# Optimization experiments

Hardware: AMD Instinct MI355X
Metric: run time of the kernel (lower is better)

## Reference

```python
import jax, jax.numpy as jnp
import numpy as np

BETA = 1.0
DEPTH = 10
LEVELS = DEPTH - 1          # decision levels along any root->leaf path
NUM_LEAVES = 2 ** LEVELS    # 512
NUM_INTERNAL = NUM_LEAVES - 1  # 511, heap-ordered: root=0, children 2i+1/2i+2


def _tree_paths():
    """For each leaf, the heap indices of its ancestors and the branch taken (0=left,1=right)."""
    anc = np.zeros((NUM_LEAVES, LEVELS), dtype=np.int32)
    bits = np.zeros((NUM_LEAVES, LEVELS), dtype=np.int32)
    for j in range(NUM_LEAVES):
        node = 0
        for t in range(LEVELS):
            bit = (j >> (LEVELS - 1 - t)) & 1
            anc[j, t] = node
            bits[j, t] = bit
            node = 2 * node + 1 + bit
    return jnp.asarray(anc), jnp.asarray(bits)

_ANC, _BITS = _tree_paths()


def setup_inputs() -> dict:
    key = jax.random.key(0)
    k1, k2, k3, k4 = jax.random.split(key, 4)
    B, F, K = 8192, 4096, 1000
    return {
        "xs": jax.random.normal(k1, (B, F), dtype=jnp.float32),
        "W": jax.random.normal(k2, (NUM_INTERNAL, F), dtype=jnp.float32) * (1.0 / np.sqrt(F)),
        "b": jax.random.normal(k3, (NUM_INTERNAL,), dtype=jnp.float32) * 0.01,
        "leaf_params": jax.random.normal(k4, (NUM_LEAVES, K), dtype=jnp.float32),
    }


def reference(xs, W, b, leaf_params):
    # All node projections as one GEMM: [B, NUM_INTERNAL]
    ps = jax.nn.sigmoid(BETA * (xs @ W.T + b))
    # Gather per-leaf ancestor probs: [B, NUM_LEAVES, LEVELS]
    g = ps[:, _ANC]
    edge = jnp.where(_BITS[None] == 1, g, 1.0 - g)
    leaf_prob = jnp.prod(edge, axis=-1)          # [B, NUM_LEAVES]
    dists = jax.nn.softmax(leaf_params, axis=-1)  # [NUM_LEAVES, K]
    return leaf_prob @ dists                      # [B, K]
```

## Files before the change

kernel.cpp:

```cpp
#include <hip/hip_runtime.h>


typedef __bf16 bf16x8 __attribute__((ext_vector_type(8)));
typedef float f32x4 __attribute__((ext_vector_type(4)));
typedef _Float16 f16x8 __attribute__((ext_vector_type(8)));

#define B_DIM 8192
#define F_DIM 4096
#define NI 511
#define NL 512
#define K_DIM 1000
#define KPAD 1024
#define SPLIT 3

#define W_BLKS  1024
#define SM_BLKS 512

__device__ inline unsigned short f2bf(float f) {
    unsigned int u = __float_as_uint(f);
    return (unsigned short)((u + 0x7FFFu + ((u >> 16) & 1u)) >> 16);
}
__device__ inline unsigned int pk_bf16(float a, float b) {
    return (unsigned int)f2bf(a) | ((unsigned int)f2bf(b) << 16);
}
__device__ inline unsigned int pk2_hu(float a, float b) {
    unsigned int ua = __float_as_uint(a) + 0x8000u;
    unsigned int ub = __float_as_uint(b) + 0x8000u;
    return __builtin_amdgcn_perm(ub, ua, 0x07060302u);
}

typedef __attribute__((address_space(1))) const unsigned int guint;
typedef __attribute__((address_space(3))) unsigned int luint;
__device__ inline void gload16(const unsigned short* g, unsigned short* l) {
    __builtin_amdgcn_global_load_lds((guint*)g, (luint*)l, 16, 0, 0);
}

__device__ inline bf16x8 ldb(const unsigned short* Lbase, int r, int kb) {
    const int g = (kb >> 3) ^ (r & 7);
    return *(const bf16x8*)&Lbase[r * 64 + g * 8];
}

__device__ inline float waveMax(float v) {
#pragma unroll
    for (int off = 32; off; off >>= 1) v = fmaxf(v, __shfl_down(v, off, 64));
    return v;
}
__device__ inline float waveSum(float v) {
#pragma unroll
    for (int off = 32; off; off >>= 1) v += __shfl_down(v, off, 64);
    return v;
}

__global__ __launch_bounds__(256) void prep_kernel(
    const float* __restrict__ W, unsigned short* __restrict__ Wb,
    const float* __restrict__ lp, unsigned short* __restrict__ dT)
{
    __shared__ float sred[8];
    const int bid = blockIdx.x;
    const int tid = threadIdx.x;

    if (bid < W_BLKS) {
        const size_t i = ((size_t)bid * 256 + tid) * 8;
        const int row = (int)(i >> 12);
        uint4 h = {0u, 0u, 0u, 0u};
        if (row < NI) {
            const float4 a = *(const float4*)(W + i);
            const float4 b = *(const float4*)(W + i + 4);
            h.x = pk_bf16(a.x, a.y);
            h.y = pk_bf16(a.z, a.w);
            h.z = pk_bf16(b.x, b.y);
            h.w = pk_bf16(b.z, b.w);
        }
        *(uint4*)(Wb + i) = h;
        return;
    }
    const int k = bid - W_BLKS;
    const int lane = tid & 63;
    const int wave = tid >> 6;
    const float* rowp = lp + (size_t)k * K_DIM;

    float vals[4];
    float mx = -3.0e38f;
#pragma unroll
    for (int c = 0; c < 4; ++c) {
        const int n = tid + c * 256;
        vals[c] = (n < K_DIM) ? rowp[n] : -3.0e38f;
        mx = fmaxf(mx, vals[c]);
    }
    mx = waveMax(mx);
    if (lane == 0) sred[wave] = mx;
    __syncthreads();
    const float gmax = fmaxf(fmaxf(sred[0], sred[1]), fmaxf(sred[2], sred[3]));

    float sum = 0.f;
#pragma unroll
    for (int c = 0; c < 4; ++c) {
        const int n = tid + c * 256;
        const float e = (n < K_DIM) ? __expf(vals[c] - gmax) : 0.f;
        vals[c] = e;
        sum += e;
    }
    sum = waveSum(sum);
    if (lane == 0) sred[4 + wave] = sum;
    __syncthreads();
    const float inv = 1.0f / (sred[4] + sred[5] + sred[6] + sred[7]);
#pragma unroll
    for (int c = 0; c < 4; ++c) {
        const int n = tid + c * 256;
        if (n < K_DIM) dT[(size_t)n * NL + k] = f2bf(vals[c] * inv);
    }
}

__global__ __launch_bounds__(256) __attribute__((amdgpu_waves_per_eu(3, 3)))
void gemm1_kernel(
    const float* __restrict__ A, const unsigned short* __restrict__ Bb,
    _Float16* __restrict__ part)
{
    __shared__ __align__(16) unsigned short Al[128 * 64];
    __shared__ __align__(16) unsigned short Bl[2][128 * 64];

    const int id = blockIdx.x;
    const int xcd = id & 7;
    const int j = id >> 3;
    const int nt = j & 3;
    const int rem = j >> 2;
    const int mhi = rem / 3;
    const int z = rem - mhi * 3;
    const int m0 = (mhi * 8 + xcd) * 128;
    const int n0 = nt * 128;
    const int kbeg = z * 1408;
    const int NT = (z == 2) ? 20 : 22;

    const int tid = threadIdx.x;
    const int lane = tid & 63;
    const int wave = tid >> 6;
    const int wm = (wave >> 1) * 64;
    const int wn = (wave & 1) * 64;
    const int quad = lane >> 4;
    const int l16 = lane & 15;

    const int rowA = wave * 4 + (lane >> 4);
    const int q = lane & 15;
    const float* gA = A + (size_t)(m0 + rowA) * F_DIM + kbeg + q * 4;
    unsigned short* lw[8];
#pragma unroll
    for (int p = 0; p < 8; ++p) {
        const int r = rowA + p * 16;
        lw[p] = &Al[r * 64 + (((q >> 1) ^ (r & 7)) * 8) + (q & 1) * 4];
    }

    const int drb = lane >> 3;
    const int cb = ((lane & 7) ^ drb) * 8;
    const unsigned short* gB = Bb + (size_t)(n0 + wave * 8 + drb) * F_DIM + kbeg + cb;
    const int lBoff = wave * 8 * 64;

    const f32x4 zero = {0.f, 0.f, 0.f, 0.f};
    f32x4 acc[4][4];
#pragma unroll
    for (int i = 0; i < 4; ++i)
#pragma unroll
        for (int j2 = 0; j2 < 4; ++j2) acc[i][j2] = zero;

    f32x4 abf[8];
    uint2 abh[8];

#pragma unroll
    for (int p = 0; p < 4; ++p)
        gload16(gB + (size_t)p * 32 * F_DIM, &Bl[0][lBoff + p * 2048]);
    __builtin_amdgcn_sched_barrier(0);
#pragma unroll
    for (int p = 0; p < 8; ++p)
        abf[p] = *(const f32x4*)(gA + (size_t)p * 16 * F_DIM);
    __builtin_amdgcn_sched_barrier(0);
#pragma unroll
    for (int p = 0; p < 8; ++p) {
        abh[p].x = pk2_hu(abf[p].x, abf[p].y);
        abh[p].y = pk2_hu(abf[p].z, abf[p].w);
    }
#pragma unroll
    for (int p = 0; p < 8; ++p)
        abf[p] = *(const f32x4*)(gA + 64 + (size_t)p * 16 * F_DIM);
    __builtin_amdgcn_sched_barrier(0);

    for (int t = 0; t < NT; ++t) {
#pragma unroll
        for (int p = 0; p < 8; ++p)
            *(uint2*)lw[p] = abh[p];
        if (t < NT - 1) {
            asm volatile("s_waitcnt vmcnt(8) lgkmcnt(0)" ::: "memory");
        } else {
            asm volatile("s_waitcnt vmcnt(0) lgkmcnt(0)" ::: "memory");
        }
        __builtin_amdgcn_sched_barrier(0);
        __builtin_amdgcn_s_barrier();
        __builtin_amdgcn_sched_barrier(0);
        if (t + 1 < NT) {
#pragma unroll
            for (int p = 0; p < 4; ++p)
                gload16(gB + (size_t)(t + 1) * 64 + (size_t)p * 32 * F_DIM,
                        &Bl[(t + 1) & 1][lBoff + p * 2048]);
        }
        __builtin_amdgcn_sched_barrier(0);
        if (t + 1 < NT) {
#pragma unroll
            for (int p = 0; p < 8; ++p) {
                abh[p].x = pk2_hu(abf[p].x, abf[p].y);
                abh[p].y = pk2_hu(abf[p].z, abf[p].w);
            }
        }
        if (t + 2 < NT) {
#pragma unroll
            for (int p = 0; p < 8; ++p)
                abf[p] = *(const f32x4*)(gA + (size_t)(t + 2) * 64
                                         + (size_t)p * 16 * F_DIM);
        }
        __builtin_amdgcn_sched_barrier(0);
        const unsigned short* Bcur = &Bl[t & 1][0];
#pragma unroll
        for (int kk = 0; kk < 64; kk += 32) {
            const int kb = kk + quad * 8;
            bf16x8 av[4], bv[4];
#pragma unroll
            for (int i = 0; i < 4; ++i)
                av[i] = ldb(Al, wm + i * 16 + l16, kb);
#pragma unroll
            for (int j2 = 0; j2 < 4; ++j2)
                bv[j2] = ldb(Bcur, wn + j2 * 16 + l16, kb);
#pragma unroll
            for (int i = 0; i < 4; ++i)
#pragma unroll
                for (int j2 = 0; j2 < 4; ++j2)
                    acc[i][j2] = __builtin_amdgcn_mfma_f32_16x16x32_bf16(
                        av[i], bv[j2], acc[i][j2], 0, 0, 0);
        }
        __builtin_amdgcn_sched_barrier(0);
        __builtin_amdgcn_s_barrier();
        __builtin_amdgcn_sched_barrier(0);
    }

    _Float16* dst = part + (size_t)z * ((size_t)B_DIM * NL);
#pragma unroll
    for (int i = 0; i < 4; ++i) {
        const int mbase = m0 + wm + i * 16 + quad * 4;
#pragma unroll
        for (int j2 = 0; j2 < 4; ++j2) {
            const int n = n0 + wn + j2 * 16 + l16;
#pragma unroll
            for (int r = 0; r < 4; ++r)
                dst[(size_t)(mbase + r) * NL + n] = (_Float16)acc[i][j2][r];
        }
    }
}

__global__ __launch_bounds__(256) void reduce_tree_kernel(
    const _Float16* __restrict__ part, const float* __restrict__ bvec,
    unsigned short* __restrict__ leafbf)
{
    __shared__ float bsh[NL];
    __shared__ float prow[4][NL];

    const int tid = threadIdx.x;
    bsh[tid] = (tid < NI) ? bvec[tid] : 0.0f;
    const int t2 = tid + 256;
    bsh[t2] = (t2 < NI) ? bvec[t2] : 0.0f;

    const int wave = tid >> 6;
    const int lane = tid & 63;
    const int row = blockIdx.x * 4 + wave;
    const size_t base = (size_t)row * NL + lane * 8;

    float v[8] = {0.f, 0.f, 0.f, 0.f, 0.f, 0.f, 0.f, 0.f};
#pragma unroll
    for (int s = 0; s < SPLIT; ++s) {
        const f16x8 h = *(const f16x8*)(part + (size_t)s * ((size_t)B_DIM * NL) + base);
#pragma unroll
        for (int e = 0; e < 8; ++e) v[e] += (float)h[e];
    }
    __syncthreads();

#pragma unroll
    for (int i = 0; i < 8; ++i) {
        const float x = v[i] + bsh[lane * 8 + i];
        prow[wave][lane * 8 + i] = 1.0f / (1.0f + __expf(-x));
    }
    __syncthreads();

    const float* pr = prow[wave];
    float pre = 1.0f;
    int pnode = 0;
#pragma unroll
    for (int t = 5; t >= 0; --t) {
        const int bit = (lane >> t) & 1;
        const float p = pr[pnode];
        pre *= bit ? p : (1.0f - p);
        pnode = 2 * pnode + 1 + bit;
    }
    unsigned short outs[8];
#pragma unroll
    for (int jj = 0; jj < 8; ++jj) {
        float prob = pre;
        int node = pnode;
#pragma unroll
        for (int t = 2; t >= 0; --t) {
            const int bit = (jj >> t) & 1;
            const float p = pr[node];
            prob *= bit ? p : (1.0f - p);
            node = 2 * node + 1 + bit;
        }
        outs[jj] = f2bf(prob);
    }
    uint4 r;
    r.x = (unsigned int)outs[0] | ((unsigned int)outs[1] << 16);
    r.y = (unsigned int)outs[2] | ((unsigned int)outs[3] << 16);
    r.z = (unsigned int)outs[4] | ((unsigned int)outs[5] << 16);
    r.w = (unsigned int)outs[6] | ((unsigned int)outs[7] << 16);
    *(uint4*)(leafbf + (size_t)row * NL + lane * 8) = r;
}

__global__ __launch_bounds__(256, 2) void gemm2_kernel(
    const unsigned short* __restrict__ A, const unsigned short* __restrict__ Bm,
    float* __restrict__ out)
{
    __shared__ __align__(16) unsigned short Al[2][128 * 64];
    __shared__ __align__(16) unsigned short Bl[2][128 * 64];

    const int id = blockIdx.x;
    const int xcd = id & 7;
    const int j = id >> 3;
    const int nt = j & 7;
    const int mhi = j >> 3;
    const int m0 = (mhi * 8 + xcd) * 128;
    const int n0 = nt * 128;

    const int tid = threadIdx.x;
    const int lane = tid & 63;
    const int wave = tid >> 6;
    const int wm = (wave >> 1) * 64;
    const int wn = (wave & 1) * 64;
    const int quad = lane >> 4;
    const int l16 = lane & 15;

    const int drb = lane >> 3;
    const int cb = ((lane & 7) ^ drb) * 8;
    const unsigned short* gA = A + (size_t)(m0 + wave * 8 + drb) * NL + cb;
    const unsigned short* gB = Bm + (size_t)(n0 + wave * 8 + drb) * NL + cb;
    const int loff = wave * 8 * 64;

    const f32x4 zero = {0.f, 0.f, 0.f, 0.f};
    f32x4 acc[4][4];
#pragma unroll
    for (int i = 0; i < 4; ++i)
#pragma unroll
        for (int j2 = 0; j2 < 4; ++j2) acc[i][j2] = zero;

#pragma unroll
    for (int p = 0; p < 4; ++p) {
        gload16(gA + (size_t)p * 32 * NL, &Al[0][loff + p * 2048]);
        gload16(gB + (size_t)p * 32 * NL, &Bl[0][loff + p * 2048]);
    }
    __builtin_amdgcn_sched_barrier(0);

#pragma unroll
    for (int t = 0; t < 8; ++t) {
        if (t + 1 < 8) {
#pragma unroll
            for (int p = 0; p < 4; ++p) {
                gload16(gA + (size_t)(t + 1) * 64 + (size_t)p * 32 * NL,
                        &Al[(t + 1) & 1][loff + p * 2048]);
                gload16(gB + (size_t)(t + 1) * 64 + (size_t)p * 32 * NL,
                        &Bl[(t + 1) & 1][loff + p * 2048]);
            }
            __builtin_amdgcn_sched_barrier(0);
            asm volatile("s_waitcnt vmcnt(8)" ::: "memory");
        } else {
            __builtin_amdgcn_sched_barrier(0);
            asm volatile("s_waitcnt vmcnt(0)" ::: "memory");
        }
        __builtin_amdgcn_sched_barrier(0);
        __builtin_amdgcn_s_barrier();
        __builtin_amdgcn_sched_barrier(0);
#pragma unroll
        for (int kk = 0; kk < 64; kk += 32) {
            const int kb = kk + quad * 8;
            bf16x8 av[4], bv[4];
#pragma unroll
            for (int i = 0; i < 4; ++i)
                av[i] = ldb(&Al[t & 1][0], wm + i * 16 + l16, kb);
#pragma unroll
            for (int j2 = 0; j2 < 4; ++j2)
                bv[j2] = ldb(&Bl[t & 1][0], wn + j2 * 16 + l16, kb);
#pragma unroll
            for (int i = 0; i < 4; ++i)
#pragma unroll
                for (int j2 = 0; j2 < 4; ++j2)
                    acc[i][j2] = __builtin_amdgcn_mfma_f32_16x16x32_bf16(av[i], bv[j2], acc[i][j2], 0, 0, 0);
        }
        __builtin_amdgcn_sched_barrier(0);
        __builtin_amdgcn_s_barrier();
        __builtin_amdgcn_sched_barrier(0);
    }

#pragma unroll
    for (int i = 0; i < 4; ++i) {
        const int mbase = m0 + wm + i * 16 + quad * 4;
#pragma unroll
        for (int j2 = 0; j2 < 4; ++j2) {
            const int n = n0 + wn + j2 * 16 + l16;
            if (n < K_DIM) {
#pragma unroll
                for (int r = 0; r < 4; ++r)
                    out[(size_t)(mbase + r) * K_DIM + n] = acc[i][j2][r];
            }
        }
    }
}

extern "C" void kernel_launch(void* const* d_in, const int* in_sizes, int n_in,
                              void* d_out, int out_size, void* d_ws, size_t ws_size,
                              hipStream_t stream) {
    const float* xs = (const float*)d_in[0];
    const float* W  = (const float*)d_in[1];
    const float* b  = (const float*)d_in[2];
    const float* lp = (const float*)d_in[3];
    float* out = (float*)d_out;

    const size_t partB = (size_t)B_DIM * NL * 2;
    const size_t leafB = (size_t)B_DIM * NL * 2;
    const size_t dTB   = (size_t)KPAD * NL * 2;

    char* ws = (char*)d_ws;
    _Float16* part = (_Float16*)ws;
    unsigned short* leafbf = (unsigned short*)(ws + SPLIT * partB);
    unsigned short* dT = (unsigned short*)(ws + SPLIT * partB + leafB);
    unsigned short* Wb = (unsigned short*)(ws + SPLIT * partB + leafB + dTB);
    (void)ws_size;

    hipLaunchKernelGGL(prep_kernel, dim3(W_BLKS + SM_BLKS), dim3(256), 0, stream,
                       W, Wb, lp, dT);
    hipLaunchKernelGGL(gemm1_kernel, dim3(768), dim3(256), 0, stream,
                       xs, Wb, part);
    hipLaunchKernelGGL(reduce_tree_kernel, dim3(B_DIM / 4), dim3(256), 0, stream,
                       part, b, leafbf);
    hipLaunchKernelGGL(gemm2_kernel, dim3(8 * 8 * 8), dim3(256), 0, stream,
                       leafbf, dT, out);
}
```

Measured before the change: 264.8 us.

## Widen gemm1 block tile to full N and use four-way split-K

Each gemm1 block now covers all 512 output columns with 512 threads (128x512 tile) instead of 128 columns, and split-K changes from three to four even chunks of 1024. As a result each fp32 row of xs is loaded and converted to bf16 only once rather than once per N tile, which removes most of the redundant A traffic and conversion work. The cost is a larger LDS footprint (about 144KB for double-buffered B), more accumulator registers per wave, only 256 blocks with one per CU, and one extra partial-sum buffer for the reduction kernel to read.

New measurement: 258.9 us. -2.2%, faster.

```diff
diff --git a/kernel.cpp b/kernel.cpp
--- a/kernel.cpp
+++ b/kernel.cpp
@@ -11,7 +11,7 @@
 #define NL 512
 #define K_DIM 1000
 #define KPAD 1024
-#define SPLIT 3
+#define SPLIT 4
 
 #define W_BLKS  1024
 #define SM_BLKS 512
@@ -111,83 +111,80 @@
     }
 }
 
-__global__ __launch_bounds__(256) __attribute__((amdgpu_waves_per_eu(3, 3)))
+__global__ __launch_bounds__(512) __attribute__((amdgpu_waves_per_eu(2, 2)))
 void gemm1_kernel(
     const float* __restrict__ A, const unsigned short* __restrict__ Bb,
     _Float16* __restrict__ part)
 {
     __shared__ __align__(16) unsigned short Al[128 * 64];
-    __shared__ __align__(16) unsigned short Bl[2][128 * 64];
+    __shared__ __align__(16) unsigned short Bl[2][512 * 64];
 
     const int id = blockIdx.x;
     const int xcd = id & 7;
-    const int j = id >> 3;
-    const int nt = j & 3;
-    const int rem = j >> 2;
-    const int mhi = rem / 3;
-    const int z = rem - mhi * 3;
-    const int m0 = (mhi * 8 + xcd) * 128;
-    const int n0 = nt * 128;
-    const int kbeg = z * 1408;
-    const int NT = (z == 2) ? 20 : 22;
+    const int g = id >> 3;
+    const int mt = xcd * 8 + (g >> 2);
+    const int z = g & 3;
+    const int m0 = mt * 128;
+    const int kbeg = z * 1024;
+    const int NT = 16;
 
     const int tid = threadIdx.x;
     const int lane = tid & 63;
     const int wave = tid >> 6;
-    const int wm = (wave >> 1) * 64;
-    const int wn = (wave & 1) * 64;
+    const int wm = (wave >> 2) * 64;
+    const int wn = (wave & 3) * 128;
     const int quad = lane >> 4;
     const int l16 = lane & 15;
 
     const int rowA = wave * 4 + (lane >> 4);
     const int q = lane & 15;
     const float* gA = A + (size_t)(m0 + rowA) * F_DIM + kbeg + q * 4;
-    unsigned short* lw[8];
-#pragma unroll
-    for (int p = 0; p < 8; ++p) {
-        const int r = rowA + p * 16;
+    unsigned short* lw[4];
+#pragma unroll
+    for (int p = 0; p < 4; ++p) {
+        const int r = rowA + p * 32;
         lw[p] = &Al[r * 64 + (((q >> 1) ^ (r & 7)) * 8) + (q & 1) * 4];
     }
 
     const int drb = lane >> 3;
     const int cb = ((lane & 7) ^ drb) * 8;
-    const unsigned short* gB = Bb + (size_t)(n0 + wave * 8 + drb) * F_DIM + kbeg + cb;
+    const unsigned short* gB = Bb + (size_t)(wave * 8 + drb) * F_DIM + kbeg + cb;
     const int lBoff = wave * 8 * 64;
 
     const f32x4 zero = {0.f, 0.f, 0.f, 0.f};
-    f32x4 acc[4][4];
+    f32x4 acc[4][8];
 #pragma unroll
     for (int i = 0; i < 4; ++i)
 #pragma unroll
-        for (int j2 = 0; j2 < 4; ++j2) acc[i][j2] = zero;
-
-    f32x4 abf[8];
-    uint2 abh[8];
-
+        for (int j2 = 0; j2 < 8; ++j2) acc[i][j2] = zero;
+
+    f32x4 abf[4];
+    uint2 abh[4];
+
+#pragma unroll
+    for (int p = 0; p < 8; ++p)
+        gload16(gB + (size_t)p * 64 * F_DIM, &Bl[0][p * 4096 + lBoff]);
+    __builtin_amdgcn_sched_barrier(0);
 #pragma unroll
     for (int p = 0; p < 4; ++p)
-        gload16(gB + (size_t)p * 32 * F_DIM, &Bl[0][lBoff + p * 2048]);
+        abf[p] = *(const f32x4*)(gA + (size_t)p * 32 * F_DIM);
     __builtin_amdgcn_sched_barrier(0);
 #pragma unroll
-    for (int p = 0; p < 8; ++p)
-        abf[p] = *(const f32x4*)(gA + (size_t)p * 16 * F_DIM);
-    __builtin_amdgcn_sched_barrier(0);
-#pragma unroll
-    for (int p = 0; p < 8; ++p) {
+    for (int p = 0; p < 4; ++p) {
         abh[p].x = pk2_hu(abf[p].x, abf[p].y);
         abh[p].y = pk2_hu(abf[p].z, abf[p].w);
     }
 #pragma unroll
-    for (int p = 0; p < 8; ++p)
-        abf[p] = *(const f32x4*)(gA + 64 + (size_t)p * 16 * F_DIM);
+    for (int p = 0; p < 4; ++p)
+        abf[p] = *(const f32x4*)(gA + 64 + (size_t)p * 32 * F_DIM);
     __builtin_amdgcn_sched_barrier(0);
 
     for (int t = 0; t < NT; ++t) {
 #pragma unroll
-        for (int p = 0; p < 8; ++p)
+        for (int p = 0; p < 4; ++p)
             *(uint2*)lw[p] = abh[p];
         if (t < NT - 1) {
-            asm volatile("s_waitcnt vmcnt(8) lgkmcnt(0)" ::: "memory");
+            asm volatile("s_waitcnt vmcnt(4) lgkmcnt(0)" ::: "memory");
         } else {
             asm volatile("s_waitcnt vmcnt(0) lgkmcnt(0)" ::: "memory");
         }
@@ -196,42 +193,41 @@
         __builtin_amdgcn_sched_barrier(0);
         if (t + 1 < NT) {
 #pragma unroll
-            for (int p = 0; p < 4; ++p)
-                gload16(gB + (size_t)(t + 1) * 64 + (size_t)p * 32 * F_DIM,
-                        &Bl[(t + 1) & 1][lBoff + p * 2048]);
+            for (int p = 0; p < 8; ++p)
+                gload16(gB + (size_t)(t + 1) * 64 + (size_t)p * 64 * F_DIM,
+                        &Bl[(t + 1) & 1][p * 4096 + lBoff]);
         }
         __builtin_amdgcn_sched_barrier(0);
         if (t + 1 < NT) {
 #pragma unroll
-            for (int p = 0; p < 8; ++p) {
+            for (int p = 0; p < 4; ++p) {
                 abh[p].x = pk2_hu(abf[p].x, abf[p].y);
                 abh[p].y = pk2_hu(abf[p].z, abf[p].w);
             }
         }
         if (t + 2 < NT) {
 #pragma unroll
-            for (int p = 0; p < 8; ++p)
+            for (int p = 0; p < 4; ++p)
                 abf[p] = *(const f32x4*)(gA + (size_t)(t + 2) * 64
-                                         + (size_t)p * 16 * F_DIM);
+                                         + (size_t)p * 32 * F_DIM);
         }
         __builtin_amdgcn_sched_barrier(0);
         const unsigned short* Bcur = &Bl[t & 1][0];
 #pragma unroll
         for (int kk = 0; kk < 64; kk += 32) {
             const int kb = kk + quad * 8;
-            bf16x8 av[4], bv[4];
+            bf16x8 av[4];
 #pragma unroll
             for (int i = 0; i < 4; ++i)
                 av[i] = ldb(Al, wm + i * 16 + l16, kb);
 #pragma unroll
-            for (int j2 = 0; j2 < 4; ++j2)
-                bv[j2] = ldb(Bcur, wn + j2 * 16 + l16, kb);
-#pragma unroll
-            for (int i = 0; i < 4; ++i)
-#pragma unroll
-                for (int j2 = 0; j2 < 4; ++j2)
+            for (int j2 = 0; j2 < 8; ++j2) {
+                const bf16x8 bv = ldb(Bcur, wn + j2 * 16 + l16, kb);
+#pragma unroll
+                for (int i = 0; i < 4; ++i)
                     acc[i][j2] = __builtin_amdgcn_mfma_f32_16x16x32_bf16(
-                        av[i], bv[j2], acc[i][j2], 0, 0, 0);
+                        av[i], bv, acc[i][j2], 0, 0, 0);
+            }
         }
         __builtin_amdgcn_sched_barrier(0);
         __builtin_amdgcn_s_barrier();
@@ -243,8 +239,8 @@
     for (int i = 0; i < 4; ++i) {
         const int mbase = m0 + wm + i * 16 + quad * 4;
 #pragma unroll
-        for (int j2 = 0; j2 < 4; ++j2) {
-            const int n = n0 + wn + j2 * 16 + l16;
+        for (int j2 = 0; j2 < 8; ++j2) {
+            const int n = wn + j2 * 16 + l16;
 #pragma unroll
             for (int r = 0; r < 4; ++r)
                 dst[(size_t)(mbase + r) * NL + n] = (_Float16)acc[i][j2][r];
@@ -437,7 +433,7 @@
 
     hipLaunchKernelGGL(prep_kernel, dim3(W_BLKS + SM_BLKS), dim3(256), 0, stream,
                        W, Wb, lp, dT);
-    hipLaunchKernelGGL(gemm1_kernel, dim3(768), dim3(256), 0, stream,
+    hipLaunchKernelGGL(gemm1_kernel, dim3(256), dim3(512), 0, stream,
                        xs, Wb, part);
     hipLaunchKernelGGL(reduce_tree_kernel, dim3(B_DIM / 4), dim3(256), 0, stream,
                        part, b, leafbf);
```
